# Optimization experiments

Measured on AMD Instinct MI355X. Metric: run time of the kernel, lower is better.

The kernel has to match this reference:

```python
import jax, jax.numpy as jnp
import numpy as np
import math

DIM = 1024
NHEADS = 8
HEAD_DIM = 128
MAXSEQLEN = 2048
THETA = 10000.0


def _rope_tables():
    # speed = theta ** (-(arange(0, dim, 2) / dim)), t = arange(maxseqlen)
    half = HEAD_DIM // 2
    speed = THETA ** (-(np.arange(0, HEAD_DIM, 2)[:half].astype(np.float32) / HEAD_DIM))
    t = np.arange(MAXSEQLEN, dtype=np.float32)
    freqs = np.outer(t, speed)  # [maxseqlen, head_dim//2]
    return jnp.asarray(np.cos(freqs)), jnp.asarray(np.sin(freqs))


def setup_inputs() -> dict:
    key = jax.random.key(0)
    kx, kqkv, kout = jax.random.split(key, 3)
    B, T = 2, 2048
    hdim = NHEADS * HEAD_DIM
    std = 0.5 * DIM ** (-0.5)
    bound = (3.0 ** 0.5) * std
    x = jax.random.normal(kx, (B, T, DIM), dtype=jnp.float32)
    qkv_proj = jax.random.uniform(kqkv, (3, hdim, DIM), dtype=jnp.float32,
                                  minval=-bound, maxval=bound)
    # nn.Linear(hdim, dim, bias=False) default init: U(-1/sqrt(hdim), 1/sqrt(hdim))
    wb = 1.0 / math.sqrt(hdim)
    w_out = jax.random.uniform(kout, (DIM, hdim), dtype=jnp.float32,
                               minval=-wb, maxval=wb)
    cos, sin = _rope_tables()
    return {"x": x, "qkv_proj": qkv_proj, "w_out": w_out, "cos": cos, "sin": sin}


def _apply_rope(u, cos, sin):
    # u: [B, T, H, D]; rotate adjacent pairs (complex multiply)
    B, T, H, D = u.shape
    u = u.reshape(B, T, H, D // 2, 2)
    c = cos[:T][None, :, None, :]  # [1, T, 1, D//2]
    s = sin[:T][None, :, None, :]
    re = u[..., 0] * c - u[..., 1] * s
    im = u[..., 0] * s + u[..., 1] * c
    return jnp.stack([re, im], axis=-1).reshape(B, T, H, D)


def reference(x, qkv_proj, w_out, cos, sin):
    B, T, D = x.shape
    # fused QKV projection: [B, T, 3, hdim] -> [B, T, 3, H, head_dim]
    qkv = jnp.einsum('btd,ahd->btah', x, qkv_proj)
    qkv = qkv.reshape(B, T, 3, NHEADS, HEAD_DIM)
    q, k, v = qkv[:, :, 0], qkv[:, :, 1], qkv[:, :, 2]
    q = _apply_rope(q, cos, sin)
    k = _apply_rope(k, cos, sin)
    scale = HEAD_DIM ** (-0.5)
    logits = jnp.einsum('btnh,bsnh->bnts', q, k) * scale  # [B, H, T, T]
    causal = jnp.tril(jnp.ones((T, T), dtype=bool))
    masked = jnp.where(causal[None, None], logits, -jnp.inf)
    attn = jax.nn.softmax(masked, axis=-1)
    out = jnp.einsum('bnts,bsnh->btnh', attn, v).reshape(B, T, -1)
    out = out @ w_out.T  # [B, T, dim]
    return out, attn
```

## Files before the change

kernel.cpp:

```cpp
#include <hip/hip_runtime.h>

typedef __attribute__((ext_vector_type(8))) short bf16x8;
typedef __attribute__((ext_vector_type(4))) short bf16x4;
typedef __attribute__((ext_vector_type(4))) float f32x4;

#define MFMA(a, b, c) __builtin_amdgcn_mfma_f32_16x16x32_bf16((a), (b), (c), 0, 0, 0)

__device__ __forceinline__ unsigned short f2bf(float f) {
  unsigned int x = __float_as_uint(f);
  return (unsigned short)((x + 0x7fffu + ((x >> 16) & 1u)) >> 16);
}
__device__ __forceinline__ unsigned int cvtpk(float lo, float hi) {
  unsigned int r;
  asm("v_cvt_pk_bf16_f32 %0, %1, %2" : "=v"(r) : "v"(lo), "v"(hi));
  return r;
}

constexpr int SEQ = 2048;
constexpr int NH = 8;
constexpr int DH = 128;
constexpr int DIM = 1024;
constexpr float SCALE = 0.08838834764831845f;

__global__ __launch_bounds__(256) void k_qkv_rope(
    const float* __restrict__ x, const float* __restrict__ wqkv,
    const float* __restrict__ cosT, const float* __restrict__ sinT,
    unsigned short* __restrict__ q, unsigned short* __restrict__ k,
    unsigned short* __restrict__ vT)
{
  __shared__ __align__(16) unsigned short As[128][40];
  __shared__ __align__(16) unsigned short Bs[128][40];
  const int tid = threadIdx.x;
  const int wave = tid >> 6, lane = tid & 63;
  const int fr = lane & 15, fq = lane >> 4;
  const int fk = fq * 8;
  const int wr = (wave >> 1) * 64, wc = (wave & 1) * 64;
  const int m0 = blockIdx.x * 128, n0 = blockIdx.y * 128;

  f32x4 zero4 = {0.f, 0.f, 0.f, 0.f};
  f32x4 acc[4][4];
  for (int i = 0; i < 4; ++i)
    for (int j = 0; j < 4; ++j) acc[i][j] = zero4;

  for (int kt = 0; kt < 32; ++kt) {
    const int k0 = kt * 32;
    __syncthreads();
#pragma unroll
    for (int j = 0; j < 4; ++j) {
      int f = j * 256 + tid;
      int row = f >> 3, c4 = (f & 7) * 4;
      f32x4 va = *(const f32x4*)(x + (m0 + row) * 1024 + k0 + c4);
      f32x4 vb = *(const f32x4*)(wqkv + (n0 + row) * 1024 + k0 + c4);
      uint2 ua, ub;
      ua.x = cvtpk(va[0], va[1]); ua.y = cvtpk(va[2], va[3]);
      ub.x = cvtpk(vb[0], vb[1]); ub.y = cvtpk(vb[2], vb[3]);
      *(uint2*)&As[row][c4] = ua;
      *(uint2*)&Bs[row][c4] = ub;
    }
    __syncthreads();
    bf16x8 af[4], bfr[4];
#pragma unroll
    for (int mi = 0; mi < 4; ++mi) af[mi] = *(const bf16x8*)&As[wr + mi * 16 + fr][fk];
#pragma unroll
    for (int ni = 0; ni < 4; ++ni) bfr[ni] = *(const bf16x8*)&Bs[wc + ni * 16 + fr][fk];
#pragma unroll
    for (int mi = 0; mi < 4; ++mi)
#pragma unroll
      for (int ni = 0; ni < 4; ++ni)
        acc[mi][ni] = MFMA(af[mi], bfr[ni], acc[mi][ni]);
  }

#pragma unroll
  for (int mi = 0; mi < 4; ++mi)
#pragma unroll
    for (int ni = 0; ni < 4; ++ni)
#pragma unroll
      for (int r = 0; r < 4; ++r) {
        float val = acc[mi][ni][r];
        float other = __shfl_xor(val, 1, 64);
        int m = m0 + wr + mi * 16 + fq * 4 + r;
        int n = n0 + wc + ni * 16 + fr;
        int a = n >> 10, feat = n & 1023;
        int hh = feat >> 7, dh = feat & 127;
        int bi = m >> 11, t = m & 2047;
        if (a == 2) {
          vT[((bi * NH + hh) * DH + dh) * SEQ + t] = f2bf(val);
        } else {
          float c = cosT[t * 64 + (dh >> 1)];
          float s = sinT[t * 64 + (dh >> 1)];
          float o = ((dh & 1) == 0) ? (val * c - other * s) : (other * s + val * c);
          unsigned short* dst = (a == 0) ? q : k;
          dst[((bi * NH + hh) * SEQ + t) * DH + dh] = f2bf(o);
        }
      }
}

__global__ __launch_bounds__(256) void k_attn(
    const unsigned short* __restrict__ q, const unsigned short* __restrict__ k,
    const unsigned short* __restrict__ vT,
    float* __restrict__ attn, unsigned short* __restrict__ heads)
{
  __shared__ __align__(16) unsigned short Kt[64][140];
  __shared__ __align__(16) unsigned short Vt[128][76];
  __shared__ __align__(16) unsigned short Esc[4][16][76];

  const int tid = threadIdx.x;
  const int wave = tid >> 6, lane = tid & 63;
  const int fr = lane & 15, fq = lane >> 4;
  const int fk = fq * 8;
  const int rt = (blockIdx.z == 0) ? (int)blockIdx.x : (31 - (int)blockIdx.x);
  const int row0 = rt * 64;
  const int hh = blockIdx.y, bi = blockIdx.z;
  const int bh = bi * NH + hh;
  const int r0 = row0 + wave * 16;

  const unsigned short* qb = q + bh * SEQ * DH;
  const unsigned short* kb = k + bh * SEQ * DH;
  const unsigned short* vb = vT + bh * DH * SEQ;

  bf16x8 aq[4];
#pragma unroll
  for (int ks = 0; ks < 4; ++ks)
    aq[ks] = *(const bf16x8*)(qb + (r0 + fr) * DH + ks * 32 + fk);

  const int wmax = r0 + 15;
  float rs[4] = {0.f, 0.f, 0.f, 0.f};

  for (int nt = 0; nt <= rt; ++nt) {
    const int c0 = nt * 64;
    __syncthreads();
#pragma unroll
    for (int j = 0; j < 4; ++j) {
      int f = j * 256 + tid;
      int r = f >> 4, c = (f & 15) * 8;
      *(bf16x8*)&Kt[r][c] = *(const bf16x8*)(kb + (c0 + r) * DH + c);
    }
    __syncthreads();
#pragma unroll
    for (int half = 0; half < 4; ++half) {
      int ch = c0 + half * 16;
      if (ch <= wmax) {
        f32x4 s = {0.f, 0.f, 0.f, 0.f};
#pragma unroll
        for (int ks = 0; ks < 4; ++ks) {
          bf16x8 bk = *(const bf16x8*)&Kt[half * 16 + fr][ks * 32 + fk];
          s = MFMA(aq[ks], bk, s);
        }
        int col = ch + fr;
#pragma unroll
        for (int r = 0; r < 4; ++r) {
          int row = r0 + fq * 4 + r;
          if (col <= row) rs[r] += __expf(s[r] * SCALE);
        }
      }
    }
  }

#pragma unroll
  for (int r = 0; r < 4; ++r)
#pragma unroll
    for (int msk = 1; msk < 16; msk <<= 1)
      rs[r] += __shfl_xor(rs[r], msk, 64);

  float inv[4];
#pragma unroll
  for (int r = 0; r < 4; ++r) inv[r] = 1.0f / rs[r];

  f32x4 pv[8];
  {
    f32x4 zero4 = {0.f, 0.f, 0.f, 0.f};
#pragma unroll
    for (int i = 0; i < 8; ++i) pv[i] = zero4;
  }

  for (int nt = 0; nt <= rt; ++nt) {
    const int c0 = nt * 64;
    __syncthreads();
#pragma unroll
    for (int j = 0; j < 4; ++j) {
      int f = j * 256 + tid;
      int r = f >> 4, c = (f & 15) * 8;
      *(bf16x8*)&Kt[r][c] = *(const bf16x8*)(kb + (c0 + r) * DH + c);
      int rv = f >> 3, cv = (f & 7) * 8;
      *(bf16x8*)&Vt[rv][cv] = *(const bf16x8*)(vb + rv * SEQ + c0 + cv);
    }
    __syncthreads();
#pragma unroll
    for (int half = 0; half < 4; ++half) {
      int ch = c0 + half * 16;
      bool live = (ch <= wmax);
      f32x4 s = {0.f, 0.f, 0.f, 0.f};
      if (live) {
#pragma unroll
        for (int ks = 0; ks < 4; ++ks) {
          bf16x8 bk = *(const bf16x8*)&Kt[half * 16 + fr][ks * 32 + fk];
          s = MFMA(aq[ks], bk, s);
        }
      }
      int col = ch + fr;
#pragma unroll
      for (int r = 0; r < 4; ++r) {
        int row = r0 + fq * 4 + r;
        float p = (live && col <= row) ? __expf(s[r] * SCALE) * inv[r] : 0.f;
        attn[((size_t)bh * SEQ + row) * SEQ + col] = p;
        Esc[wave][fq * 4 + r][half * 16 + fr] = f2bf(p);
      }
    }
    bf16x8 ae0 = *(const bf16x8*)&Esc[wave][fr][fk];
    bf16x8 ae1 = *(const bf16x8*)&Esc[wave][fr][32 + fk];
#pragma unroll
    for (int ni = 0; ni < 8; ++ni) {
      bf16x8 bv0 = *(const bf16x8*)&Vt[ni * 16 + fr][fk];
      bf16x8 bv1 = *(const bf16x8*)&Vt[ni * 16 + fr][32 + fk];
      pv[ni] = MFMA(ae0, bv0, pv[ni]);
      pv[ni] = MFMA(ae1, bv1, pv[ni]);
    }
  }

#pragma unroll
  for (int ni = 0; ni < 8; ++ni)
#pragma unroll
    for (int r = 0; r < 4; ++r) {
      int row = r0 + fq * 4 + r;
      int dh = ni * 16 + fr;
      heads[(bi * SEQ + row) * DIM + hh * DH + dh] = f2bf(pv[ni][r]);
    }

  {
    const int zstart = row0 + 64;
    f32x4 z4 = {0.f, 0.f, 0.f, 0.f};
#pragma unroll
    for (int rr = 0; rr < 4; ++rr) {
      int row = r0 + rr * 4 + fq;
      float* dst = attn + ((size_t)bh * SEQ + row) * SEQ;
      for (int c = zstart + fr * 4; c < SEQ; c += 64)
        *(f32x4*)(dst + c) = z4;
    }
  }
}

__global__ __launch_bounds__(256) void k_outproj(
    const unsigned short* __restrict__ heads, const float* __restrict__ wout,
    float* __restrict__ out)
{
  __shared__ __align__(16) unsigned short As[128][40];
  __shared__ __align__(16) unsigned short Bs[128][40];
  const int tid = threadIdx.x;
  const int wave = tid >> 6, lane = tid & 63;
  const int fr = lane & 15, fq = lane >> 4;
  const int fk = fq * 8;
  const int wr = (wave >> 1) * 64, wc = (wave & 1) * 64;
  const int m0 = blockIdx.x * 128, n0 = blockIdx.y * 128;

  f32x4 zero4 = {0.f, 0.f, 0.f, 0.f};
  f32x4 acc[4][4];
  for (int i = 0; i < 4; ++i)
    for (int j = 0; j < 4; ++j) acc[i][j] = zero4;

  for (int kt = 0; kt < 32; ++kt) {
    const int k0 = kt * 32;
    __syncthreads();
#pragma unroll
    for (int j = 0; j < 2; ++j) {
      int f = j * 256 + tid;
      int row = f >> 2, c = (f & 3) * 8;
      *(bf16x8*)&As[row][c] = *(const bf16x8*)(heads + (m0 + row) * 1024 + k0 + c);
    }
#pragma unroll
    for (int j = 0; j < 4; ++j) {
      int f = j * 256 + tid;
      int row = f >> 3, c4 = (f & 7) * 4;
      f32x4 vb = *(const f32x4*)(wout + (n0 + row) * 1024 + k0 + c4);
      uint2 ub;
      ub.x = cvtpk(vb[0], vb[1]); ub.y = cvtpk(vb[2], vb[3]);
      *(uint2*)&Bs[row][c4] = ub;
    }
    __syncthreads();
    bf16x8 af[4], bfr[4];
#pragma unroll
    for (int mi = 0; mi < 4; ++mi) af[mi] = *(const bf16x8*)&As[wr + mi * 16 + fr][fk];
#pragma unroll
    for (int ni = 0; ni < 4; ++ni) bfr[ni] = *(const bf16x8*)&Bs[wc + ni * 16 + fr][fk];
#pragma unroll
    for (int mi = 0; mi < 4; ++mi)
#pragma unroll
      for (int ni = 0; ni < 4; ++ni)
        acc[mi][ni] = MFMA(af[mi], bfr[ni], acc[mi][ni]);
  }

#pragma unroll
  for (int mi = 0; mi < 4; ++mi)
#pragma unroll
    for (int ni = 0; ni < 4; ++ni)
#pragma unroll
      for (int r = 0; r < 4; ++r) {
        int m = m0 + wr + mi * 16 + fq * 4 + r;
        int n = n0 + wc + ni * 16 + fr;
        out[m * 1024 + n] = acc[mi][ni][r];
      }
}

extern "C" void kernel_launch(void* const* d_in, const int* in_sizes, int n_in,
                              void* d_out, int out_size, void* d_ws, size_t ws_size,
                              hipStream_t stream)
{
  const float* x    = (const float*)d_in[0];
  const float* wqkv = (const float*)d_in[1];
  const float* wout = (const float*)d_in[2];
  const float* cosT = (const float*)d_in[3];
  const float* sinT = (const float*)d_in[4];

  float* out  = (float*)d_out;
  float* attn = out + 4194304;
  unsigned short* ws   = (unsigned short*)d_ws;
  unsigned short* q     = ws;
  unsigned short* kk    = ws + 4194304;
  unsigned short* vT    = ws + 8388608;
  unsigned short* heads = ws + 12582912;

  k_qkv_rope<<<dim3(32, 24), 256, 0, stream>>>(x, wqkv, cosT, sinT, q, kk, vT);
  k_attn<<<dim3(32, 8, 2), 256, 0, stream>>>(q, kk, vT, attn, heads);
  k_outproj<<<dim3(32, 8), 256, 0, stream>>>(heads, wout, out);
}
```

Baseline: 219.7 us.

## Split attention KV tiles across two wave groups per block with LDS reduction

The attention kernel now runs 512 threads per block. Two groups of four waves each take alternating 64-column KV tiles, so each block loads 128 columns of K and V per iteration. Row sums and PV accumulators from the two groups are combined through shared memory before normalizing and writing heads. This doubles the parallelism per row tile to hide latency on the long causal rows. The cost is a larger LDS footprint (about 80KB), extra barriers and a cross-group reduction, and the odd group idles on the last super-tile when the tile count is odd.

```diff
diff --git a/kernel.cpp b/kernel.cpp
--- a/kernel.cpp
+++ b/kernel.cpp
@@ -95,62 +95,76 @@
       }
 }
 
-__global__ __launch_bounds__(256) void k_attn(
+__global__ __launch_bounds__(512, 4) void k_attn(
     const unsigned short* __restrict__ q, const unsigned short* __restrict__ k,
     const unsigned short* __restrict__ vT,
     float* __restrict__ attn, unsigned short* __restrict__ heads)
 {
-  __shared__ __align__(16) unsigned short Kt[64][140];
-  __shared__ __align__(16) unsigned short Vt[128][76];
-  __shared__ __align__(16) unsigned short Esc[4][16][76];
+  __shared__ __align__(16) char smem[80384];
+  unsigned short* KtE  = (unsigned short*)(smem);
+  unsigned short* KtO  = (unsigned short*)(smem + 17408);
+  unsigned short* VtE  = (unsigned short*)(smem + 34816);
+  unsigned short* VtO  = (unsigned short*)(smem + 52224);
+  unsigned short* EscB = (unsigned short*)(smem + 69632);
+  float* rsbuf = (float*)(smem + 79872);
+  float* pvscr = (float*)(smem);
 
   const int tid = threadIdx.x;
   const int wave = tid >> 6, lane = tid & 63;
   const int fr = lane & 15, fq = lane >> 4;
   const int fk = fq * 8;
+  const int hi = wave >> 2;
   const int rt = (blockIdx.z == 0) ? (int)blockIdx.x : (31 - (int)blockIdx.x);
   const int row0 = rt * 64;
   const int hh = blockIdx.y, bi = blockIdx.z;
   const int bh = bi * NH + hh;
-  const int r0 = row0 + wave * 16;
+  const int r0 = row0 + (wave & 3) * 16;
+  const int wmax = r0 + 15;
 
   const unsigned short* qb = q + bh * SEQ * DH;
   const unsigned short* kb = k + bh * SEQ * DH;
   const unsigned short* vb = vT + bh * DH * SEQ;
 
+  unsigned short* myK = hi ? KtO : KtE;
+  unsigned short* myV = hi ? VtO : VtE;
+  unsigned short* myEsc = EscB + wave * (16 * 40);
+
   bf16x8 aq[4];
 #pragma unroll
   for (int ks = 0; ks < 4; ++ks)
     aq[ks] = *(const bf16x8*)(qb + (r0 + fr) * DH + ks * 32 + fk);
 
-  const int wmax = r0 + 15;
+  const int nsuper = (rt >> 1) + 1;
   float rs[4] = {0.f, 0.f, 0.f, 0.f};
 
-  for (int nt = 0; nt <= rt; ++nt) {
-    const int c0 = nt * 64;
-    __syncthreads();
-#pragma unroll
-    for (int j = 0; j < 4; ++j) {
-      int f = j * 256 + tid;
+  for (int si = 0; si < nsuper; ++si) {
+    const int cE = si * 128;
+    __syncthreads();
+#pragma unroll
+    for (int j = 0; j < 2; ++j) {
+      int f = j * 512 + tid;
       int r = f >> 4, c = (f & 15) * 8;
-      *(bf16x8*)&Kt[r][c] = *(const bf16x8*)(kb + (c0 + r) * DH + c);
-    }
-    __syncthreads();
-#pragma unroll
-    for (int half = 0; half < 4; ++half) {
-      int ch = c0 + half * 16;
-      if (ch <= wmax) {
-        f32x4 s = {0.f, 0.f, 0.f, 0.f};
-#pragma unroll
-        for (int ks = 0; ks < 4; ++ks) {
-          bf16x8 bk = *(const bf16x8*)&Kt[half * 16 + fr][ks * 32 + fk];
-          s = MFMA(aq[ks], bk, s);
-        }
-        int col = ch + fr;
-#pragma unroll
-        for (int r = 0; r < 4; ++r) {
-          int row = r0 + fq * 4 + r;
-          if (col <= row) rs[r] += __expf(s[r] * SCALE);
+      *(bf16x8*)&KtE[r * 136 + c] = *(const bf16x8*)(kb + (cE + r) * DH + c);
+      *(bf16x8*)&KtO[r * 136 + c] = *(const bf16x8*)(kb + (cE + 64 + r) * DH + c);
+    }
+    __syncthreads();
+    const int myT = 2 * si + hi;
+    if (myT <= rt) {
+      const int c0 = myT * 64;
+#pragma unroll
+      for (int half = 0; half < 4; ++half) {
+        int ch = c0 + half * 16;
+        if (ch <= wmax) {
+          f32x4 s = {0.f, 0.f, 0.f, 0.f};
+#pragma unroll
+          for (int ks = 0; ks < 4; ++ks) {
+            bf16x8 bk = *(const bf16x8*)&myK[(half * 16 + fr) * 136 + ks * 32 + fk];
+            s = MFMA(aq[ks], bk, s);
+          }
+          int col = ch + fr;
+#pragma unroll
+          for (int r = 0; r < 4; ++r)
+            if (col <= r0 + fq * 4 + r) rs[r] += __expf(s[r] * SCALE);
         }
       }
     }
@@ -162,9 +176,16 @@
     for (int msk = 1; msk < 16; msk <<= 1)
       rs[r] += __shfl_xor(rs[r], msk, 64);
 
+  __syncthreads();
+  if (fr == 0) {
+#pragma unroll
+    for (int r = 0; r < 4; ++r) rsbuf[wave * 16 + fq * 4 + r] = rs[r];
+  }
+  __syncthreads();
   float inv[4];
 #pragma unroll
-  for (int r = 0; r < 4; ++r) inv[r] = 1.0f / rs[r];
+  for (int r = 0; r < 4; ++r)
+    inv[r] = 1.0f / (rs[r] + rsbuf[(wave ^ 4) * 16 + fq * 4 + r]);
 
   f32x4 pv[8];
   {
@@ -173,64 +194,91 @@
     for (int i = 0; i < 8; ++i) pv[i] = zero4;
   }
 
-  for (int nt = 0; nt <= rt; ++nt) {
-    const int c0 = nt * 64;
-    __syncthreads();
-#pragma unroll
-    for (int j = 0; j < 4; ++j) {
-      int f = j * 256 + tid;
+  for (int si = 0; si < nsuper; ++si) {
+    const int cE = si * 128;
+    __syncthreads();
+#pragma unroll
+    for (int j = 0; j < 2; ++j) {
+      int f = j * 512 + tid;
       int r = f >> 4, c = (f & 15) * 8;
-      *(bf16x8*)&Kt[r][c] = *(const bf16x8*)(kb + (c0 + r) * DH + c);
+      *(bf16x8*)&KtE[r * 136 + c] = *(const bf16x8*)(kb + (cE + r) * DH + c);
+      *(bf16x8*)&KtO[r * 136 + c] = *(const bf16x8*)(kb + (cE + 64 + r) * DH + c);
       int rv = f >> 3, cv = (f & 7) * 8;
-      *(bf16x8*)&Vt[rv][cv] = *(const bf16x8*)(vb + rv * SEQ + c0 + cv);
-    }
-    __syncthreads();
-#pragma unroll
-    for (int half = 0; half < 4; ++half) {
-      int ch = c0 + half * 16;
-      bool live = (ch <= wmax);
-      f32x4 s = {0.f, 0.f, 0.f, 0.f};
-      if (live) {
-#pragma unroll
-        for (int ks = 0; ks < 4; ++ks) {
-          bf16x8 bk = *(const bf16x8*)&Kt[half * 16 + fr][ks * 32 + fk];
-          s = MFMA(aq[ks], bk, s);
+      *(bf16x8*)&VtE[rv * 68 + cv] = *(const bf16x8*)(vb + rv * SEQ + cE + cv);
+      *(bf16x8*)&VtO[rv * 68 + cv] = *(const bf16x8*)(vb + rv * SEQ + cE + 64 + cv);
+    }
+    __syncthreads();
+    const int myT = 2 * si + hi;
+    if (myT <= rt) {
+      const int c0 = myT * 64;
+#pragma unroll
+      for (int chunk = 0; chunk < 2; ++chunk) {
+#pragma unroll
+        for (int h2 = 0; h2 < 2; ++h2) {
+          const int half = chunk * 2 + h2;
+          const int ch = c0 + half * 16;
+          const bool live = (ch <= wmax);
+          f32x4 s = {0.f, 0.f, 0.f, 0.f};
+          if (live) {
+#pragma unroll
+            for (int ks = 0; ks < 4; ++ks) {
+              bf16x8 bk = *(const bf16x8*)&myK[(half * 16 + fr) * 136 + ks * 32 + fk];
+              s = MFMA(aq[ks], bk, s);
+            }
+          }
+          const int col = ch + fr;
+#pragma unroll
+          for (int r = 0; r < 4; ++r) {
+            int row = r0 + fq * 4 + r;
+            float p = (live && col <= row) ? __expf(s[r] * SCALE) * inv[r] : 0.f;
+            attn[((size_t)bh * SEQ + row) * SEQ + col] = p;
+            myEsc[(fq * 4 + r) * 40 + h2 * 16 + fr] = f2bf(p);
+          }
         }
-      }
-      int col = ch + fr;
+        bf16x8 ae = *(const bf16x8*)&myEsc[fr * 40 + fk];
+#pragma unroll
+        for (int ni = 0; ni < 8; ++ni) {
+          bf16x8 bv = *(const bf16x8*)&myV[(ni * 16 + fr) * 68 + chunk * 32 + fk];
+          pv[ni] = MFMA(ae, bv, pv[ni]);
+        }
+      }
+    }
+  }
+
+  __syncthreads();
+  {
+    const int pair = wave & 3;
+    float* wdst = pvscr + (pair * 2 + 1 - hi) * (16 * 66);
+#pragma unroll
+    for (int n4 = 0; n4 < 4; ++n4) {
+      int ni = (1 - hi) * 4 + n4;
+#pragma unroll
+      for (int r = 0; r < 4; ++r)
+        wdst[(fq * 4 + r) * 66 + n4 * 16 + fr] = pv[ni][r];
+    }
+  }
+  __syncthreads();
+  {
+    const int pair = wave & 3;
+    const float* rsrc = pvscr + (pair * 2 + hi) * (16 * 66);
+#pragma unroll
+    for (int n4 = 0; n4 < 4; ++n4) {
+      int ni = hi * 4 + n4;
 #pragma unroll
       for (int r = 0; r < 4; ++r) {
+        float v = pv[ni][r] + rsrc[(fq * 4 + r) * 66 + n4 * 16 + fr];
         int row = r0 + fq * 4 + r;
-        float p = (live && col <= row) ? __expf(s[r] * SCALE) * inv[r] : 0.f;
-        attn[((size_t)bh * SEQ + row) * SEQ + col] = p;
-        Esc[wave][fq * 4 + r][half * 16 + fr] = f2bf(p);
-      }
-    }
-    bf16x8 ae0 = *(const bf16x8*)&Esc[wave][fr][fk];
-    bf16x8 ae1 = *(const bf16x8*)&Esc[wave][fr][32 + fk];
-#pragma unroll
-    for (int ni = 0; ni < 8; ++ni) {
-      bf16x8 bv0 = *(const bf16x8*)&Vt[ni * 16 + fr][fk];
-      bf16x8 bv1 = *(const bf16x8*)&Vt[ni * 16 + fr][32 + fk];
-      pv[ni] = MFMA(ae0, bv0, pv[ni]);
-      pv[ni] = MFMA(ae1, bv1, pv[ni]);
-    }
-  }
-
-#pragma unroll
-  for (int ni = 0; ni < 8; ++ni)
-#pragma unroll
-    for (int r = 0; r < 4; ++r) {
-      int row = r0 + fq * 4 + r;
-      int dh = ni * 16 + fr;
-      heads[(bi * SEQ + row) * DIM + hh * DH + dh] = f2bf(pv[ni][r]);
-    }
+        int dh = ni * 16 + fr;
+        heads[(bi * SEQ + row) * DIM + hh * DH + dh] = f2bf(v);
+      }
+    }
+  }
 
   {
     const int zstart = row0 + 64;
     f32x4 z4 = {0.f, 0.f, 0.f, 0.f};
 #pragma unroll
-    for (int rr = 0; rr < 4; ++rr) {
+    for (int rr = hi * 2; rr < hi * 2 + 2; ++rr) {
       int row = r0 + rr * 4 + fq;
       float* dst = attn + ((size_t)bh * SEQ + row) * SEQ;
       for (int c = zstart + fr * 4; c < SEQ; c += 64)
@@ -312,13 +360,13 @@
 
   float* out  = (float*)d_out;
   float* attn = out + 4194304;
-  unsigned short* ws   = (unsigned short*)d_ws;
+  unsigned short* ws = (unsigned short*)d_ws;
   unsigned short* q     = ws;
   unsigned short* kk    = ws + 4194304;
   unsigned short* vT    = ws + 8388608;
   unsigned short* heads = ws + 12582912;
 
   k_qkv_rope<<<dim3(32, 24), 256, 0, stream>>>(x, wqkv, cosT, sinT, q, kk, vT);
-  k_attn<<<dim3(32, 8, 2), 256, 0, stream>>>(q, kk, vT, attn, heads);
+  k_attn<<<dim3(32, 8, 2), 512, 0, stream>>>(q, kk, vT, attn, heads);
   k_outproj<<<dim3(32, 8), 256, 0, stream>>>(heads, wout, out);
 }
```

After: 285.8 us. +30.1%, slower.
